# Performance work log

Hardware: AMD Instinct MI355X
Metric: run time of the kernel (lower is better)

The kernel has to match this reference:

```python
import jax, jax.numpy as jnp
import numpy as np

N, D = 4096, 128  # seq length / feature dim of x is N; head dim is D

def setup_inputs() -> dict:
    key = jax.random.key(0)
    k1, k2 = jax.random.split(key)
    x = jax.random.normal(k1, (N, N), dtype=jnp.float32)
    # nn.Linear(N, 3*d): weight [3d, N], bias [3d]; scale weight like torch init
    W = jax.random.normal(k2, (3 * D, N), dtype=jnp.float32) / jnp.sqrt(jnp.float32(N))
    b = jnp.zeros((3 * D,), dtype=jnp.float32)
    return {"x": x, "W": W, "b": b}

def reference(x, W, b):
    # QKV projection: [N, 3d]
    qkv = x @ W.T + b
    Q, K, V = jnp.split(qkv, 3, axis=-1)  # each [N, d]
    # The blockwise online-softmax double loop computes exactly
    # softmax(Q K^T) V with NO 1/sqrt(d) scaling (faithful to source).
    S = Q @ K.T                 # [N, N]
    P = jax.nn.softmax(S, axis=-1)
    return P @ V                # [N, d]
```

## Files before the change

### kernel.cpp

```cpp
#include <hip/hip_runtime.h>
#include <cstdint>
#include <cstddef>

typedef _Float16 f16;
typedef f16 f16x8 __attribute__((ext_vector_type(8)));
typedef f16 f16x4 __attribute__((ext_vector_type(4)));
typedef float f32x4 __attribute__((ext_vector_type(4)));

#define SEQ 4096
#define DH 128
#define QKV_LD 384
#define LOG2E 1.44269504f
#define DEFER_THR 4.0f
#define SPLITS 4
#define GBM 32

__device__ __forceinline__ float fast_exp2(float x) {
#if __has_builtin(__builtin_amdgcn_exp2f)
  return __builtin_amdgcn_exp2f(x);
#else
  return exp2f(x);
#endif
}

__device__ __forceinline__ void gl_lds16(const void* g, void* l) {
  __builtin_amdgcn_global_load_lds((const __attribute__((address_space(1))) void*)g,
                                   (__attribute__((address_space(3))) void*)l, 16, 0, 0);
}

__global__ __launch_bounds__(256) void cvt_w_kernel(const float4* __restrict__ W,
                                                    f16x4* __restrict__ Wh) {
  int i = blockIdx.x * 256 + threadIdx.x;
  float4 v = W[i];
  f16x4 h; h[0] = (f16)v.x; h[1] = (f16)v.y; h[2] = (f16)v.z; h[3] = (f16)v.w;
  Wh[i] = h;
}

__global__ __launch_bounds__(256, 2) void gemm_qkv(const float* __restrict__ x,
                                                   const f16* __restrict__ Wh,
                                                   f16* __restrict__ part) {
  __shared__ __align__(16) f16 Ax[GBM][72];
  __shared__ __align__(16) f16 Bx[QKV_LD * 64];
  const int m0 = blockIdx.x * GBM;
  const int split = blockIdx.y;
  const int kc = SEQ / SPLITS;
  const int k0 = split * kc;
  const int tid = threadIdx.x;
  const int lane = tid & 63;
  const int wave = tid >> 6;
  const int nb = wave * 96;
  const int l15 = lane & 15, quad = lane >> 4;

  f32x4 acc[2][6] = {};
  float4 areg[2];

#define LOAD_A(KT)                                                         \
  do {                                                                     \
    _Pragma("unroll") for (int r = 0; r < 2; ++r) {                        \
      int c = r * 256 + tid;                                               \
      int row = c >> 4, col = (c & 15) * 4;                                \
      areg[r] = *(const float4*)&x[(size_t)(m0 + row) * SEQ + (KT) + col]; \
    }                                                                      \
  } while (0)

  LOAD_A(k0);

  for (int kt = k0; kt < k0 + kc; kt += 64) {
#pragma unroll
    for (int r = 0; r < 12; ++r) {
      int c = r * 256 + tid;
      int row = c >> 3, ch = c & 7;
      const f16* src = &Wh[(size_t)row * SEQ + kt + ((ch ^ (row & 7)) << 3)];
      gl_lds16(src, &Bx[(size_t)c << 3]);
    }
#pragma unroll
    for (int r = 0; r < 2; ++r) {
      int c = r * 256 + tid;
      int row = c >> 4, col = (c & 15) * 4;
      f16x4 h; h[0] = (f16)areg[r].x; h[1] = (f16)areg[r].y;
      h[2] = (f16)areg[r].z; h[3] = (f16)areg[r].w;
      *(f16x4*)&Ax[row][col] = h;
    }
    __syncthreads();
    if (kt + 64 < k0 + kc) LOAD_A(kt + 64);
#pragma unroll
    for (int ks = 0; ks < 2; ++ks) {
      f16x8 a[2], bb[6];
#pragma unroll
      for (int t = 0; t < 2; ++t)
        a[t] = *(const f16x8*)&Ax[t * 16 + l15][ks * 32 + quad * 8];
#pragma unroll
      for (int t = 0; t < 6; ++t) {
        int n = nb + t * 16 + l15;
        int ch = (ks * 4 + quad) ^ (l15 & 7);
        bb[t] = *(const f16x8*)&Bx[((size_t)n << 6) + (ch << 3)];
      }
#pragma unroll
      for (int mt = 0; mt < 2; ++mt)
#pragma unroll
        for (int nt = 0; nt < 6; ++nt)
          acc[mt][nt] = __builtin_amdgcn_mfma_f32_16x16x32_f16(a[mt], bb[nt], acc[mt][nt], 0, 0, 0);
    }
    __syncthreads();
  }
#undef LOAD_A

  f16* pw = part + (((size_t)split * 128 + blockIdx.x) * 12) * 256 * 4;
#pragma unroll
  for (int mt = 0; mt < 2; ++mt) {
#pragma unroll
    for (int nt = 0; nt < 6; ++nt) {
      int p = mt * 6 + nt;
      f16x4 h;
#pragma unroll
      for (int rr = 0; rr < 4; ++rr) h[rr] = (f16)acc[mt][nt][rr];
      *(f16x4*)&pw[((size_t)p * 256 + tid) * 4] = h;
    }
  }
}

__global__ __launch_bounds__(256) void reduce_qkv(const f16* __restrict__ part,
                                                  const float* __restrict__ bias,
                                                  f16* __restrict__ qkv,
                                                  f16* __restrict__ Vt) {
  __shared__ __align__(16) f16 Vl[128][40];
  const int bx = blockIdx.x;
  const int tid = threadIdx.x;
  const int lane = tid & 63, wave = tid >> 6;
  const int l15 = lane & 15, quad = lane >> 4;

#pragma unroll
  for (int mt = 0; mt < 2; ++mt) {
    const int rowbase = bx * 32 + mt * 16 + quad * 4;
#pragma unroll
    for (int nt = 0; nt < 6; ++nt) {
      const int p = mt * 6 + nt;
      float acc[4] = {0.f, 0.f, 0.f, 0.f};
#pragma unroll
      for (int s = 0; s < SPLITS; ++s) {
        f16x4 v = *(const f16x4*)&part[((((size_t)s * 128 + bx) * 12 + p) * 256 + tid) * 4];
#pragma unroll
        for (int rr = 0; rr < 4; ++rr) acc[rr] += (float)v[rr];
      }
      int col = wave * 96 + nt * 16 + l15;
      float bv = bias[col];
      if (col < 256) {
#pragma unroll
        for (int rr = 0; rr < 4; ++rr)
          qkv[(size_t)(rowbase + rr) * QKV_LD + col] = (f16)(acc[rr] + bv);
      } else {
        f16x4 h;
#pragma unroll
        for (int rr = 0; rr < 4; ++rr) h[rr] = (f16)(acc[rr] + bv);
        *(f16x4*)&Vl[col - 256][mt * 16 + quad * 4] = h;
      }
    }
  }
  __syncthreads();
  {
    int d = tid >> 1, seg = tid & 1;
    f16x8 v0 = *(const f16x8*)&Vl[d][seg * 16];
    f16x8 v1 = *(const f16x8*)&Vl[d][seg * 16 + 8];
    *(f16x8*)&Vt[(size_t)d * SEQ + bx * 32 + seg * 16] = v0;
    *(f16x8*)&Vt[(size_t)d * SEQ + bx * 32 + seg * 16 + 8] = v1;
  }
}

#define NSPLIT 16
#define KVRANGE (SEQ / NSPLIT)

__global__ __launch_bounds__(256, 2) void attn_partial(const f16* __restrict__ qkv,
                                                       const f16* __restrict__ Vt,
                                                       f16* __restrict__ Op,
                                                       float* __restrict__ ml) {
  __shared__ __align__(16) f16 smem[27136];
  f16* Ks = smem;
  f16* Vs = smem + 8704;
  f16* Ps = smem + 17920;

  const int q0 = blockIdx.x * 128;
  const int split = blockIdx.y;
  const int kv0 = split * KVRANGE;
  const int tid = threadIdx.x;
  const int lane = tid & 63, wave = tid >> 6;
  const int l15 = lane & 15, quad = lane >> 4;
  const int mbase = q0 + wave * 32;
  f16* Psw = Ps + wave * 32 * 72;

  f16x8 qf[2][4];
#pragma unroll
  for (int mt = 0; mt < 2; ++mt)
#pragma unroll
    for (int ks = 0; ks < 4; ++ks) {
      f16x8 q = *(const f16x8*)&qkv[(size_t)(mbase + mt * 16 + l15) * QKV_LD + ks * 32 + quad * 8];
      qf[mt][ks] = q * (f16)LOG2E;
    }

  f32x4 oacc[2][8] = {};
  float mrow[2] = {-1e30f, -1e30f};
  float lrow[2] = {0.f, 0.f};

  f16x8 kreg[4], vreg[4];
#define LOAD_TILE(K0)                                                                  \
  do {                                                                                 \
    _Pragma("unroll") for (int r = 0; r < 4; ++r) {                                    \
      int c = tid + r * 256;                                                           \
      int row = c >> 4, col = (c & 15) * 8;                                            \
      kreg[r] = *(const f16x8*)&qkv[(size_t)((K0) + row) * QKV_LD + DH + col];         \
    }                                                                                  \
    _Pragma("unroll") for (int r = 0; r < 4; ++r) {                                    \
      int c = tid + r * 256;                                                           \
      int row = c >> 3, col = (c & 7) * 8;                                             \
      vreg[r] = *(const f16x8*)&Vt[(size_t)row * SEQ + (K0) + col];                    \
    }                                                                                  \
  } while (0)

  LOAD_TILE(kv0);

  for (int it = 0; it < KVRANGE / 64; ++it) {
#pragma unroll
    for (int r = 0; r < 4; ++r) {
      int c = tid + r * 256;
      int row = c >> 4, col = (c & 15) * 8;
      *(f16x8*)&Ks[row * 136 + col] = kreg[r];
    }
#pragma unroll
    for (int r = 0; r < 4; ++r) {
      int c = tid + r * 256;
      int row = c >> 3, col = (c & 7) * 8;
      *(f16x8*)&Vs[row * 72 + col] = vreg[r];
    }
    __syncthreads();
    if (it + 1 < KVRANGE / 64) { int k0n = kv0 + (it + 1) * 64; LOAD_TILE(k0n); }

    f32x4 st[4][2] = {};
#pragma unroll
    for (int ks = 0; ks < 4; ++ks) {
      f16x8 kf[4];
#pragma unroll
      for (int kt = 0; kt < 4; ++kt)
        kf[kt] = *(const f16x8*)&Ks[(kt * 16 + l15) * 136 + ks * 32 + quad * 8];
#pragma unroll
      for (int kt = 0; kt < 4; ++kt)
#pragma unroll
        for (int mt = 0; mt < 2; ++mt)
          st[kt][mt] = __builtin_amdgcn_mfma_f32_16x16x32_f16(kf[kt], qf[mt][ks], st[kt][mt], 0, 0, 0);
    }

    float vmax[2];
#pragma unroll
    for (int mt = 0; mt < 2; ++mt) {
      float v = -1e30f;
#pragma unroll
      for (int kt = 0; kt < 4; ++kt)
#pragma unroll
        for (int rr = 0; rr < 4; ++rr) v = fmaxf(v, st[kt][mt][rr]);
      v = fmaxf(v, __shfl_xor(v, 16));
      v = fmaxf(v, __shfl_xor(v, 32));
      vmax[mt] = v;
    }
    bool ok = (vmax[0] <= mrow[0] + DEFER_THR) & (vmax[1] <= mrow[1] + DEFER_THR);
    if (!__all(ok)) {
      float al[2];
#pragma unroll
      for (int mt = 0; mt < 2; ++mt) {
        float mnew = fmaxf(mrow[mt], vmax[mt]);
        al[mt] = fast_exp2(mrow[mt] - mnew);
        mrow[mt] = mnew;
        lrow[mt] *= al[mt];
      }
      float alr[2][4];
#pragma unroll
      for (int mt = 0; mt < 2; ++mt)
#pragma unroll
        for (int rr = 0; rr < 4; ++rr)
          alr[mt][rr] = __shfl(al[mt], quad * 4 + rr);
#pragma unroll
      for (int mt = 0; mt < 2; ++mt)
#pragma unroll
        for (int dt = 0; dt < 8; ++dt)
#pragma unroll
          for (int rr = 0; rr < 4; ++rr)
            oacc[mt][dt][rr] *= alr[mt][rr];
    }
#pragma unroll
    for (int mt = 0; mt < 2; ++mt) {
      float ls = 0.f;
#pragma unroll
      for (int kt = 0; kt < 4; ++kt) {
        f16x4 pk;
#pragma unroll
        for (int rr = 0; rr < 4; ++rr) {
          float p = fast_exp2(st[kt][mt][rr] - mrow[mt]);
          ls += p;
          pk[rr] = (f16)p;
        }
        *(f16x4*)&Psw[(mt * 16 + l15) * 72 + kt * 16 + quad * 4] = pk;
      }
      ls += __shfl_xor(ls, 16);
      ls += __shfl_xor(ls, 32);
      lrow[mt] += ls;
    }

#pragma unroll
    for (int kk = 0; kk < 2; ++kk) {
      f16x8 pf[2];
#pragma unroll
      for (int mt = 0; mt < 2; ++mt)
        pf[mt] = *(const f16x8*)&Psw[(mt * 16 + l15) * 72 + kk * 32 + quad * 8];
#pragma unroll
      for (int dt = 0; dt < 8; ++dt) {
        f16x8 vf = *(const f16x8*)&Vs[(dt * 16 + l15) * 72 + kk * 32 + quad * 8];
#pragma unroll
        for (int mt = 0; mt < 2; ++mt)
          oacc[mt][dt] = __builtin_amdgcn_mfma_f32_16x16x32_f16(pf[mt], vf, oacc[mt][dt], 0, 0, 0);
      }
    }
    __syncthreads();
  }
#undef LOAD_TILE

  f16* Os = smem;
#pragma unroll
  for (int mt = 0; mt < 2; ++mt)
#pragma unroll
    for (int dt = 0; dt < 8; ++dt)
#pragma unroll
      for (int rr = 0; rr < 4; ++rr)
        Os[(wave * 32 + mt * 16 + quad * 4 + rr) * 136 + dt * 16 + l15] = (f16)oacc[mt][dt][rr];
  if (quad == 0) {
#pragma unroll
    for (int mt = 0; mt < 2; ++mt) {
      int row = mbase + mt * 16 + l15;
      ml[((size_t)split * SEQ + row) * 2 + 0] = mrow[mt];
      ml[((size_t)split * SEQ + row) * 2 + 1] = lrow[mt];
    }
  }
  __syncthreads();
#pragma unroll
  for (int j = 0; j < 8; ++j) {
    int c = j * 256 + tid;
    int row = c >> 4, ch = c & 15;
    f16x8 v = *(const f16x8*)&Os[row * 136 + ch * 8];
    *(f16x8*)&Op[((size_t)split * SEQ + q0 + row) * DH + ch * 8] = v;
  }
}

__global__ __launch_bounds__(256) void combine_kernel(const f16* __restrict__ Op,
                                                      const float* __restrict__ ml,
                                                      float* __restrict__ out) {
  int t = blockIdx.x * 256 + threadIdx.x;
  int base = t * 8;
  int row = base >> 7;
  float ms[NSPLIT], ls[NSPLIT];
  float M = -1e30f;
#pragma unroll
  for (int s = 0; s < NSPLIT; ++s) {
    float2 v = *(const float2*)&ml[((size_t)s * SEQ + row) * 2];
    ms[s] = v.x; ls[s] = v.y;
    M = fmaxf(M, v.x);
  }
  float L = 0.f;
  float o[8] = {};
#pragma unroll
  for (int s = 0; s < NSPLIT; ++s) {
    float w = fast_exp2(ms[s] - M);
    L += ls[s] * w;
    f16x8 v = *(const f16x8*)&Op[(size_t)s * SEQ * DH + base];
#pragma unroll
    for (int j = 0; j < 8; ++j) o[j] += w * (float)v[j];
  }
  float inv = 1.0f / L;
  float4 o0, o1;
  o0.x = o[0] * inv; o0.y = o[1] * inv; o0.z = o[2] * inv; o0.w = o[3] * inv;
  o1.x = o[4] * inv; o1.y = o[5] * inv; o1.z = o[6] * inv; o1.w = o[7] * inv;
  *(float4*)&out[base] = o0;
  *(float4*)&out[base + 4] = o1;
}

extern "C" void kernel_launch(void* const* d_in, const int* in_sizes, int n_in,
                              void* d_out, int out_size, void* d_ws, size_t ws_size,
                              hipStream_t stream) {
  const float* x = (const float*)d_in[0];
  const float* W = (const float*)d_in[1];
  const float* b = (const float*)d_in[2];
  float* out = (float*)d_out;
  char* ws = (char*)d_ws;

  f16*   Wh   = (f16*)(ws);
  f16*   qkv  = (f16*)(ws + (3u << 20));
  f16*   Vt   = (f16*)(ws + (6u << 20));
  float* ml   = (float*)(ws + (7u << 20));
  char*  scr  = ws + (7u << 20) + (1u << 19);
  f16*   part = (f16*)scr;
  f16*   Op   = (f16*)scr;

  cvt_w_kernel<<<(384 * 4096 / 4) / 256, 256, 0, stream>>>((const float4*)W, (f16x4*)Wh);
  gemm_qkv<<<dim3(SEQ / GBM, SPLITS), 256, 0, stream>>>(x, Wh, part);
  reduce_qkv<<<128, 256, 0, stream>>>(part, b, qkv, Vt);
  attn_partial<<<dim3(SEQ / 128, NSPLIT), 256, 0, stream>>>(qkv, Vt, Op, ml);
  combine_kernel<<<(SEQ * DH) / 8 / 256, 256, 0, stream>>>(Op, ml, out);
}
```

Before: 153.9 us.

## Enlarge QKV GEMM row tile to 64 and pick split-K by workspace size

The QKV projection GEMM now computes 64 rows per block instead of 32, so each staged tile of W in LDS is reused across twice as many rows. Grid size is kept up by using 8 K-splits when the workspace is large enough, and 4 otherwise. The reduce kernel is adapted to the new partial layout and transposes 64-row V tiles. The trade-off is more accumulator registers per thread, which may reduce occupancy, and, with 8 splits, more partial-sum traffic to write and then reduce.

```diff
diff --git a/kernel.cpp b/kernel.cpp
--- a/kernel.cpp
+++ b/kernel.cpp
@@ -12,8 +12,6 @@
 #define QKV_LD 384
 #define LOG2E 1.44269504f
 #define DEFER_THR 4.0f
-#define SPLITS 4
-#define GBM 32
 
 __device__ __forceinline__ float fast_exp2(float x) {
 #if __has_builtin(__builtin_amdgcn_exp2f)
@@ -36,12 +34,13 @@
   Wh[i] = h;
 }
 
+template <int SPLITS>
 __global__ __launch_bounds__(256, 2) void gemm_qkv(const float* __restrict__ x,
                                                    const f16* __restrict__ Wh,
                                                    f16* __restrict__ part) {
-  __shared__ __align__(16) f16 Ax[GBM][72];
+  __shared__ __align__(16) f16 Ax[64][72];
   __shared__ __align__(16) f16 Bx[QKV_LD * 64];
-  const int m0 = blockIdx.x * GBM;
+  const int m0 = blockIdx.x * 64;
   const int split = blockIdx.y;
   const int kc = SEQ / SPLITS;
   const int k0 = split * kc;
@@ -51,12 +50,12 @@
   const int nb = wave * 96;
   const int l15 = lane & 15, quad = lane >> 4;
 
-  f32x4 acc[2][6] = {};
-  float4 areg[2];
+  f32x4 acc[4][6] = {};
+  float4 areg[4];
 
 #define LOAD_A(KT)                                                         \
   do {                                                                     \
-    _Pragma("unroll") for (int r = 0; r < 2; ++r) {                        \
+    _Pragma("unroll") for (int r = 0; r < 4; ++r) {                        \
       int c = r * 256 + tid;                                               \
       int row = c >> 4, col = (c & 15) * 4;                                \
       areg[r] = *(const float4*)&x[(size_t)(m0 + row) * SEQ + (KT) + col]; \
@@ -74,7 +73,7 @@
       gl_lds16(src, &Bx[(size_t)c << 3]);
     }
 #pragma unroll
-    for (int r = 0; r < 2; ++r) {
+    for (int r = 0; r < 4; ++r) {
       int c = r * 256 + tid;
       int row = c >> 4, col = (c & 15) * 4;
       f16x4 h; h[0] = (f16)areg[r].x; h[1] = (f16)areg[r].y;
@@ -85,9 +84,9 @@
     if (kt + 64 < k0 + kc) LOAD_A(kt + 64);
 #pragma unroll
     for (int ks = 0; ks < 2; ++ks) {
-      f16x8 a[2], bb[6];
-#pragma unroll
-      for (int t = 0; t < 2; ++t)
+      f16x8 a[4], bb[6];
+#pragma unroll
+      for (int t = 0; t < 4; ++t)
         a[t] = *(const f16x8*)&Ax[t * 16 + l15][ks * 32 + quad * 8];
 #pragma unroll
       for (int t = 0; t < 6; ++t) {
@@ -96,7 +95,7 @@
         bb[t] = *(const f16x8*)&Bx[((size_t)n << 6) + (ch << 3)];
       }
 #pragma unroll
-      for (int mt = 0; mt < 2; ++mt)
+      for (int mt = 0; mt < 4; ++mt)
 #pragma unroll
         for (int nt = 0; nt < 6; ++nt)
           acc[mt][nt] = __builtin_amdgcn_mfma_f32_16x16x32_f16(a[mt], bb[nt], acc[mt][nt], 0, 0, 0);
@@ -105,9 +104,9 @@
   }
 #undef LOAD_A
 
-  f16* pw = part + (((size_t)split * 128 + blockIdx.x) * 12) * 256 * 4;
-#pragma unroll
-  for (int mt = 0; mt < 2; ++mt) {
+  f16* pw = part + (((size_t)split * 64 + blockIdx.x) * 24) * 256 * 4;
+#pragma unroll
+  for (int mt = 0; mt < 4; ++mt) {
 #pragma unroll
     for (int nt = 0; nt < 6; ++nt) {
       int p = mt * 6 + nt;
@@ -119,26 +118,28 @@
   }
 }
 
+template <int SPLITS>
 __global__ __launch_bounds__(256) void reduce_qkv(const f16* __restrict__ part,
                                                   const float* __restrict__ bias,
                                                   f16* __restrict__ qkv,
                                                   f16* __restrict__ Vt) {
-  __shared__ __align__(16) f16 Vl[128][40];
+  __shared__ __align__(16) f16 Vl[128][72];
   const int bx = blockIdx.x;
   const int tid = threadIdx.x;
   const int lane = tid & 63, wave = tid >> 6;
   const int l15 = lane & 15, quad = lane >> 4;
 
 #pragma unroll
-  for (int mt = 0; mt < 2; ++mt) {
-    const int rowbase = bx * 32 + mt * 16 + quad * 4;
+  for (int mt = 0; mt < 4; ++mt) {
+    const int rowl = mt * 16 + quad * 4;
+    const int rowbase = bx * 64 + rowl;
 #pragma unroll
     for (int nt = 0; nt < 6; ++nt) {
       const int p = mt * 6 + nt;
       float acc[4] = {0.f, 0.f, 0.f, 0.f};
 #pragma unroll
       for (int s = 0; s < SPLITS; ++s) {
-        f16x4 v = *(const f16x4*)&part[((((size_t)s * 128 + bx) * 12 + p) * 256 + tid) * 4];
+        f16x4 v = *(const f16x4*)&part[((((size_t)s * 64 + bx) * 24 + p) * 256 + tid) * 4];
 #pragma unroll
         for (int rr = 0; rr < 4; ++rr) acc[rr] += (float)v[rr];
       }
@@ -152,17 +153,17 @@
         f16x4 h;
 #pragma unroll
         for (int rr = 0; rr < 4; ++rr) h[rr] = (f16)(acc[rr] + bv);
-        *(f16x4*)&Vl[col - 256][mt * 16 + quad * 4] = h;
+        *(f16x4*)&Vl[col - 256][rowl] = h;
       }
     }
   }
   __syncthreads();
-  {
-    int d = tid >> 1, seg = tid & 1;
-    f16x8 v0 = *(const f16x8*)&Vl[d][seg * 16];
-    f16x8 v1 = *(const f16x8*)&Vl[d][seg * 16 + 8];
-    *(f16x8*)&Vt[(size_t)d * SEQ + bx * 32 + seg * 16] = v0;
-    *(f16x8*)&Vt[(size_t)d * SEQ + bx * 32 + seg * 16 + 8] = v1;
+#pragma unroll
+  for (int j = 0; j < 4; ++j) {
+    int c = j * 256 + tid;
+    int d = c >> 3, seg = c & 7;
+    f16x8 v = *(const f16x8*)&Vl[d][seg * 8];
+    *(f16x8*)&Vt[(size_t)d * SEQ + bx * 64 + seg * 8] = v;
   }
 }
 
@@ -396,8 +397,15 @@
   f16*   Op   = (f16*)scr;
 
   cvt_w_kernel<<<(384 * 4096 / 4) / 256, 256, 0, stream>>>((const float4*)W, (f16x4*)Wh);
-  gemm_qkv<<<dim3(SEQ / GBM, SPLITS), 256, 0, stream>>>(x, Wh, part);
-  reduce_qkv<<<128, 256, 0, stream>>>(part, b, qkv, Vt);
+
+  bool big = ws_size >= ((size_t)31u << 20) + ((size_t)1u << 19);
+  if (big) {
+    gemm_qkv<8><<<dim3(SEQ / 64, 8), 256, 0, stream>>>(x, Wh, part);
+    reduce_qkv<8><<<64, 256, 0, stream>>>(part, b, qkv, Vt);
+  } else {
+    gemm_qkv<4><<<dim3(SEQ / 64, 4), 256, 0, stream>>>(x, Wh, part);
+    reduce_qkv<4><<<64, 256, 0, stream>>>(part, b, qkv, Vt);
+  }
   attn_partial<<<dim3(SEQ / 128, NSPLIT), 256, 0, stream>>>(qkv, Vt, Op, ml);
   combine_kernel<<<(SEQ * DH) / 8 / 256, 256, 0, stream>>>(Op, ml, out);
 }
```

After: 159.7 us. 1.04x slower.
